# Optimization experiments

Hardware: AMD Instinct MI355X
Metric: run time of the kernel (lower is better)

## Reference

```python
import jax, jax.numpy as jnp
import numpy as np
from jax import lax

KH = KW = 3
STRIDE = 1
PAD = 1
B_COEF = 1.0
IN_CH = 64
OUT_CH = 64
C_LEN = 8
MLP_HIDDEN = 16


def setup_inputs() -> dict:
    key = jax.random.key(0)
    ks = jax.random.split(key, 8)
    IKK = IN_CH * KH * KW
    x = jax.random.normal(ks[0], (2, IN_CH, 32, 32), dtype=jnp.float32)
    c = jax.random.normal(ks[1], (2, C_LEN), dtype=jnp.float32)
    # static kernel [O, I*k*k] (xavier-uniform-ish)
    lim_k = float(np.sqrt(6.0 / (OUT_CH + IKK)))
    kernel = jax.random.uniform(ks[2], (OUT_CH, IKK), minval=-lim_k, maxval=lim_k, dtype=jnp.float32)
    bias = jax.random.normal(ks[3], (OUT_CH,), dtype=jnp.float32)
    # MLP: Linear(2+c_len -> 2*mlp_hidden), SiLU, Linear(2*mlp_hidden -> O*I*k*k)
    d_in = 2 + C_LEN
    d_h = 2 * MLP_HIDDEN
    lim1 = 0.1 * float(np.sqrt(6.0 / (d_in + d_h)))
    lim2 = 0.1 * float(np.sqrt(6.0 / (d_h + OUT_CH * IKK)))
    w1 = jax.random.uniform(ks[4], (d_in, d_h), minval=-lim1, maxval=lim1, dtype=jnp.float32)
    b1 = jnp.zeros((d_h,), dtype=jnp.float32)
    w2 = jax.random.uniform(ks[5], (d_h, OUT_CH * IKK), minval=-lim2, maxval=lim2, dtype=jnp.float32)
    b2 = jnp.zeros((OUT_CH * IKK,), dtype=jnp.float32)
    return {"x": x, "c": c, "kernel": kernel, "bias": bias, "w1": w1, "b1": b1, "w2": w2, "b2": b2}


def reference(x, c, kernel, bias, w1, b1, w2, b2):
    B, C, H, W = x.shape
    Ho = (H + 2 * PAD - KH) // STRIDE + 1
    Wo = (W + 2 * PAD - KW) // STRIDE + 1
    P = Ho * Wo
    O, IKK = kernel.shape
    # unfold: patches feature dim is channel-major (c, kh, kw), matching torch.nn.Unfold
    patches = lax.conv_general_dilated_patches(
        x, (KH, KW), (STRIDE, STRIDE), [(PAD, PAD), (PAD, PAD)])  # [B, IKK, Ho, Wo]
    xu = patches.reshape(B, IKK, P)  # [B, IKK, P]
    # normalized patch locations; ij-meshgrid over (x=W, y=H), flattened x-major (faithful to source)
    gx, gy = jnp.meshgrid(jnp.arange(Wo), jnp.arange(Ho), indexing='ij')
    locs = jnp.stack([gx / Wo, gy / Ho], axis=-1).reshape(-1, 2).astype(x.dtype)  # [P, 2]
    feat = jnp.concatenate(
        [jnp.broadcast_to(locs[None], (B, P, 2)),
         jnp.broadcast_to(c[:, None, :], (B, P, c.shape[1]))], axis=-1
    ).reshape(B * P, -1)  # [B*P, 2+c_len]
    h = jax.nn.silu(feat @ w1 + b1)
    adj = h @ w2 + b2  # [B*P, O*IKK]
    # faithful reshape (same raw-buffer reinterpretation as the torch .view)
    adj = adj.reshape(B, O, P, IKK).transpose(0, 1, 3, 2)  # [B, O, IKK, P]
    ak = kernel[None, :, :, None] + B_COEF * adj  # [B, O, IKK, P]
    out = jnp.einsum('bip,boip->bop', xu, ak)  # [B, O, P]
    out = out + bias[None, :, None]
    return out.reshape(B, O, Ho, Wo)
```

## Files before the change

### kernel.cpp

```cpp
#include <hip/hip_runtime.h>
#include <math.h>

#define CIN  64
#define HH   32
#define WW   32
#define OCH  64
#define IKK  576
#define DH   32
#define OIKK 36864

__device__ __forceinline__ float silu_f(float v) {
    return v / (1.0f + __expf(-v));
}

__global__ __launch_bounds__(256) void k_ts(const float* __restrict__ x,
                                            const float* __restrict__ w2,
                                            const float* __restrict__ b2,
                                            float* __restrict__ t_ws,
                                            float* __restrict__ s_ws) {
    __shared__ float patch[4][584];
    __shared__ float red[8][8][4][4];
    __shared__ float spart[4][64];
    int bid = blockIdx.x;
    int b   = bid >> 8;
    int q   = (bid >> 2) & 63;
    int ph  = bid & 3;
    int par = q >> 5, xq = q & 31;
    int tid = threadIdx.x;

    for (int idx = tid; idx < 4 * IKK; idx += 256) {
        int pgi = idx / IKK;
        int ikk = idx - pgi * IKK;
        int ci  = ikk / 9;
        int r   = ikk - ci * 9;
        int kh  = r / 3;
        int kw  = r - kh * 3;
        int yy  = 2 * (ph * 4 + pgi) + par + kh - 1;
        int xx  = xq + kw - 1;
        float v = 0.0f;
        if (yy >= 0 && yy < HH && xx >= 0 && xx < WW)
            v = x[((b * CIN + ci) * HH + yy) * WW + xx];
        patch[pgi][ikk] = v;
    }
    __syncthreads();

    int kq = tid >> 5;
    int jg = (tid >> 2) & 7;
    int pg = tid & 3;
    const float4* pr  = (const float4*)(&patch[pg][0]) + kq * 18;
    const float4* wp0 = (const float4*)(w2 + (size_t)(jg * 4 + 0) * OIKK + q * IKK) + kq * 18;
    const float4* wp1 = (const float4*)(w2 + (size_t)(jg * 4 + 1) * OIKK + q * IKK) + kq * 18;
    const float4* wp2 = (const float4*)(w2 + (size_t)(jg * 4 + 2) * OIKK + q * IKK) + kq * 18;
    const float4* wp3 = (const float4*)(w2 + (size_t)(jg * 4 + 3) * OIKK + q * IKK) + kq * 18;
    float4 a0 = {0,0,0,0}, a1 = {0,0,0,0}, a2 = {0,0,0,0}, a3 = {0,0,0,0};
    #pragma unroll 6
    for (int it = 0; it < 18; ++it) {
        float4 pv = pr[it];
        float4 w0 = wp0[it], w1v = wp1[it], w2v = wp2[it], w3v = wp3[it];
        a0.x = fmaf(w0.x, pv.x, a0.x); a0.y = fmaf(w0.y, pv.y, a0.y);
        a0.z = fmaf(w0.z, pv.z, a0.z); a0.w = fmaf(w0.w, pv.w, a0.w);
        a1.x = fmaf(w1v.x, pv.x, a1.x); a1.y = fmaf(w1v.y, pv.y, a1.y);
        a1.z = fmaf(w1v.z, pv.z, a1.z); a1.w = fmaf(w1v.w, pv.w, a1.w);
        a2.x = fmaf(w2v.x, pv.x, a2.x); a2.y = fmaf(w2v.y, pv.y, a2.y);
        a2.z = fmaf(w2v.z, pv.z, a2.z); a2.w = fmaf(w2v.w, pv.w, a2.w);
        a3.x = fmaf(w3v.x, pv.x, a3.x); a3.y = fmaf(w3v.y, pv.y, a3.y);
        a3.z = fmaf(w3v.z, pv.z, a3.z); a3.w = fmaf(w3v.w, pv.w, a3.w);
    }
    red[kq][jg][0][pg] = (a0.x + a0.y) + (a0.z + a0.w);
    red[kq][jg][1][pg] = (a1.x + a1.y) + (a1.z + a1.w);
    red[kq][jg][2][pg] = (a2.x + a2.y) + (a2.z + a2.w);
    red[kq][jg][3][pg] = (a3.x + a3.y) + (a3.z + a3.w);

    {
        int pix = tid >> 6, kc = tid & 63;
        const float* b2q = b2 + q * IKK + kc * 9;
        const float* pp  = &patch[pix][kc * 9];
        float acc = 0.f;
        #pragma unroll
        for (int i2 = 0; i2 < 9; ++i2) acc = fmaf(pp[i2], b2q[i2], acc);
        spart[pix][kc] = acc;
    }
    __syncthreads();

    if (tid < 128) {
        int j = tid >> 2, pg2 = tid & 3;
        int jg2 = j >> 2, jj2 = j & 3;
        float sum = 0.f;
        #pragma unroll
        for (int k = 0; k < 8; ++k) sum += red[k][jg2][jj2][pg2];
        int p = ((ph << 2) + pg2) * 64 + q;
        t_ws[(size_t)b * 32768 + (size_t)j * 1024 + p] = sum;
    }
    if (tid < 4) {
        float acc = 0.f;
        #pragma unroll
        for (int kc = 0; kc < 64; ++kc) acc += spart[tid][kc];
        s_ws[(b << 10) + ((ph << 2) + tid) * 64 + q] = acc;
    }
}

__global__ __launch_bounds__(256) void k_out(const float* __restrict__ x,
                                             const float* __restrict__ kern,
                                             const float* __restrict__ bias,
                                             const float* __restrict__ c,
                                             const float* __restrict__ w1,
                                             const float* __restrict__ b1,
                                             const float* __restrict__ t_ws,
                                             const float* __restrict__ s_ws,
                                             float* __restrict__ out) {
    __shared__ __align__(16) float xs[CIN][3][36];
    __shared__ __align__(16) float tl[DH][36];
    __shared__ float hl[16][33];
    __shared__ float sl[32];
    __shared__ float psum[2560];
    int bid = blockIdx.x;
    int b   = bid >> 7;
    int y   = (bid >> 2) & 31;
    int oc  = bid & 3;
    int tid = threadIdx.x;

    if (tid < 192) {
        int ci = tid / 3;
        int kh = tid - ci * 3;
        int yy = y + kh - 1;
        float4* dst = (float4*)(&xs[ci][kh][0]);
        if (yy >= 0 && yy < HH) {
            const float4* src = (const float4*)(x + ((b * CIN + ci) * HH + yy) * WW);
            float4 v[8];
            #pragma unroll
            for (int j = 0; j < 8; ++j) v[j] = src[j];
            dst[0] = make_float4(0.f, v[0].x, v[0].y, v[0].z);
            #pragma unroll
            for (int j = 1; j < 8; ++j)
                dst[j] = make_float4(v[j - 1].w, v[j].x, v[j].y, v[j].z);
            dst[8] = make_float4(v[7].w, 0.f, 0.f, 0.f);
        } else {
            float4 z = {0.f, 0.f, 0.f, 0.f};
            #pragma unroll
            for (int j = 0; j < 9; ++j) dst[j] = z;
        }
    }
    if (tid < 256) {
        int j = tid >> 3, g = tid & 7;
        float4 v = *(const float4*)(t_ws + (size_t)b * 32768 + (size_t)j * 1024 + (y << 5) + (g << 2));
        *(float4*)(&tl[j][g << 2]) = v;
    }
    for (int idx = tid; idx < 512; idx += 256) {
        int olx = idx >> 5, j = idx & 31;
        int o   = (oc << 4) + olx;
        int pm  = (o << 4) + (y >> 1);
        float f0 = (float)(pm >> 5) * (1.0f / 32.0f);
        float f1 = (float)(pm & 31) * (1.0f / 32.0f);
        float acc = b1[j];
        acc = fmaf(f0, w1[j], acc);
        acc = fmaf(f1, w1[DH + j], acc);
        #pragma unroll
        for (int i = 0; i < 8; ++i)
            acc = fmaf(c[(b << 3) + i], w1[(2 + i) * DH + j], acc);
        hl[olx][j] = silu_f(acc);
    }
    if (tid < 32) sl[tid] = s_ws[(b << 10) + (y << 5) + tid];
    __syncthreads();

    {
        int cq = tid >> 6;
        int ol = (tid >> 3) & 7;
        int xg = tid & 7;
        int o0 = (oc << 4) + ol;
        int o1 = o0 + 8;
        int ci0 = cq << 4;
        const float4* k0p = (const float4*)(kern + o0 * IKK + ci0 * 9);
        const float4* k1p = (const float4*)(kern + o1 * IKK + ci0 * 9);
        float aA[4] = {0.f, 0.f, 0.f, 0.f};
        float aB[4] = {0.f, 0.f, 0.f, 0.f};
        for (int c4 = 0; c4 < 4; ++c4) {
            float ka[36], kb[36];
            #pragma unroll
            for (int rr = 0; rr < 9; ++rr) {
                float4 va = k0p[c4 * 9 + rr];
                ka[rr * 4 + 0] = va.x; ka[rr * 4 + 1] = va.y;
                ka[rr * 4 + 2] = va.z; ka[rr * 4 + 3] = va.w;
                float4 vb = k1p[c4 * 9 + rr];
                kb[rr * 4 + 0] = vb.x; kb[rr * 4 + 1] = vb.y;
                kb[rr * 4 + 2] = vb.z; kb[rr * 4 + 3] = vb.w;
            }
            #pragma unroll
            for (int i = 0; i < 4; ++i) {
                int ci = ci0 + (c4 << 2) + i;
                #pragma unroll
                for (int kh = 0; kh < 3; ++kh) {
                    const float* row = &xs[ci][kh][0];
                    float4 v4 = *(const float4*)(row + 4 * xg);
                    float2 v2 = *(const float2*)(row + 4 * xg + 4);
                    int e = i * 9 + kh * 3;
                    float k0a = ka[e], k1a = ka[e + 1], k2a = ka[e + 2];
                    float k0b = kb[e], k1b = kb[e + 1], k2b = kb[e + 2];
                    aA[0] = fmaf(k0a, v4.x, aA[0]); aA[0] = fmaf(k1a, v4.y, aA[0]); aA[0] = fmaf(k2a, v4.z, aA[0]);
                    aA[1] = fmaf(k0a, v4.y, aA[1]); aA[1] = fmaf(k1a, v4.z, aA[1]); aA[1] = fmaf(k2a, v4.w, aA[1]);
                    aA[2] = fmaf(k0a, v4.z, aA[2]); aA[2] = fmaf(k1a, v4.w, aA[2]); aA[2] = fmaf(k2a, v2.x, aA[2]);
                    aA[3] = fmaf(k0a, v4.w, aA[3]); aA[3] = fmaf(k1a, v2.x, aA[3]); aA[3] = fmaf(k2a, v2.y, aA[3]);
                    aB[0] = fmaf(k0b, v4.x, aB[0]); aB[0] = fmaf(k1b, v4.y, aB[0]); aB[0] = fmaf(k2b, v4.z, aB[0]);
                    aB[1] = fmaf(k0b, v4.y, aB[1]); aB[1] = fmaf(k1b, v4.z, aB[1]); aB[1] = fmaf(k2b, v4.w, aB[1]);
                    aB[2] = fmaf(k0b, v4.z, aB[2]); aB[2] = fmaf(k1b, v4.w, aB[2]); aB[2] = fmaf(k2b, v2.x, aB[2]);
                    aB[3] = fmaf(k0b, v4.w, aB[3]); aB[3] = fmaf(k1b, v2.x, aB[3]); aB[3] = fmaf(k2b, v2.y, aB[3]);
                }
            }
        }
        float2* sp = (float2*)(psum + tid * 10);
        sp[0] = make_float2(aA[0], aA[1]);
        sp[1] = make_float2(aA[2], aA[3]);
        sp[2] = make_float2(aB[0], aB[1]);
        sp[3] = make_float2(aB[2], aB[3]);
    }
    __syncthreads();

    {
        int ou = tid >> 4;
        int xp = tid & 15;
        int o  = (oc << 4) + ou;
        int ol2 = ou & 7, oo = ou >> 3, xg2 = xp >> 1;
        int ppb = (xp & 1) << 1;
        float c0 = 0.f, c1 = 0.f;
        #pragma unroll
        for (int cq = 0; cq < 4; ++cq) {
            int t2 = (cq << 6) + (ol2 << 3) + xg2;
            float2 v = *(const float2*)(psum + t2 * 10 + (oo << 2) + ppb);
            c0 += v.x; c1 += v.y;
        }
        #pragma unroll 8
        for (int jj = 0; jj < DH; ++jj) {
            float2 tv = *(const float2*)(&tl[jj][2 * xp]);
            float hv = hl[ou][jj];
            c0 = fmaf(hv, tv.x, c0);
            c1 = fmaf(hv, tv.y, c1);
        }
        float bo = bias[o];
        int base = ((b * OCH + o) << 10) + (y << 5) + 2 * xp;
        *(float2*)(out + base) = make_float2(c0 + bo + sl[2 * xp], c1 + bo + sl[2 * xp + 1]);
    }
}

extern "C" void kernel_launch(void* const* d_in, const int* in_sizes, int n_in,
                              void* d_out, int out_size, void* d_ws, size_t ws_size,
                              hipStream_t stream) {
    const float* x    = (const float*)d_in[0];
    const float* c    = (const float*)d_in[1];
    const float* kern = (const float*)d_in[2];
    const float* bias = (const float*)d_in[3];
    const float* w1   = (const float*)d_in[4];
    const float* b1   = (const float*)d_in[5];
    const float* w2   = (const float*)d_in[6];
    const float* b2   = (const float*)d_in[7];
    float* out  = (float*)d_out;
    float* t_ws = (float*)d_ws;
    float* s_ws = t_ws + 65536;

    k_ts <<<512, 256, 0, stream>>>(x, w2, b2, t_ws, s_ws);
    k_out<<<256, 256, 0, stream>>>(x, kern, bias, c, w1, b1, t_ws, s_ws, out);
}
```

Measured before the change: 22.26 us.

## Fuse both kernels into one launch with a global atomic flag dependency

Merges the t/s-projection kernel and the output kernel into a single 768-block launch. The output blocks run their static-kernel convolution first, then spin on a device-scope counter until all 512 producer blocks have published, and only then consume the workspace. The goal is to remove the gap between two kernel launches and overlap the static convolution with the producer work. The cost is an extra memset per call and a spin-wait that relies on all producer blocks being scheduled, with block ordering helping to avoid deadlock.

```diff
diff --git a/kernel.cpp b/kernel.cpp
--- a/kernel.cpp
+++ b/kernel.cpp
@@ -8,235 +8,251 @@
 #define IKK  576
 #define DH   32
 #define OIKK 36864
+#define NTS  512
+
+struct TsSmem {
+    float patch[4][584];
+    float red[8][8][4][4];
+    float spart[4][64];
+};
+struct OutSmem {
+    float xs[CIN][3][36];
+    float tl[DH][36];
+    float hl[16][33];
+    float sl[32];
+    float psum[2560];
+};
+union Smem { TsSmem ts; OutSmem ot; };
 
 __device__ __forceinline__ float silu_f(float v) {
     return v / (1.0f + __expf(-v));
 }
 
-__global__ __launch_bounds__(256) void k_ts(const float* __restrict__ x,
-                                            const float* __restrict__ w2,
-                                            const float* __restrict__ b2,
-                                            float* __restrict__ t_ws,
-                                            float* __restrict__ s_ws) {
-    __shared__ float patch[4][584];
-    __shared__ float red[8][8][4][4];
-    __shared__ float spart[4][64];
+__global__ __launch_bounds__(256, 2) void k_fused(
+    const float* __restrict__ x, const float* __restrict__ c,
+    const float* __restrict__ kern, const float* __restrict__ bias,
+    const float* __restrict__ w1, const float* __restrict__ b1,
+    const float* __restrict__ w2, const float* __restrict__ b2,
+    float* __restrict__ t_ws, float* __restrict__ s_ws,
+    unsigned int* __restrict__ flag, float* __restrict__ out)
+{
+    __shared__ Smem sm;
+    int tid = threadIdx.x;
     int bid = blockIdx.x;
-    int b   = bid >> 8;
-    int q   = (bid >> 2) & 63;
-    int ph  = bid & 3;
-    int par = q >> 5, xq = q & 31;
-    int tid = threadIdx.x;
-
-    for (int idx = tid; idx < 4 * IKK; idx += 256) {
-        int pgi = idx / IKK;
-        int ikk = idx - pgi * IKK;
-        int ci  = ikk / 9;
-        int r   = ikk - ci * 9;
-        int kh  = r / 3;
-        int kw  = r - kh * 3;
-        int yy  = 2 * (ph * 4 + pgi) + par + kh - 1;
-        int xx  = xq + kw - 1;
-        float v = 0.0f;
-        if (yy >= 0 && yy < HH && xx >= 0 && xx < WW)
-            v = x[((b * CIN + ci) * HH + yy) * WW + xx];
-        patch[pgi][ikk] = v;
-    }
-    __syncthreads();
-
-    int kq = tid >> 5;
-    int jg = (tid >> 2) & 7;
-    int pg = tid & 3;
-    const float4* pr  = (const float4*)(&patch[pg][0]) + kq * 18;
-    const float4* wp0 = (const float4*)(w2 + (size_t)(jg * 4 + 0) * OIKK + q * IKK) + kq * 18;
-    const float4* wp1 = (const float4*)(w2 + (size_t)(jg * 4 + 1) * OIKK + q * IKK) + kq * 18;
-    const float4* wp2 = (const float4*)(w2 + (size_t)(jg * 4 + 2) * OIKK + q * IKK) + kq * 18;
-    const float4* wp3 = (const float4*)(w2 + (size_t)(jg * 4 + 3) * OIKK + q * IKK) + kq * 18;
-    float4 a0 = {0,0,0,0}, a1 = {0,0,0,0}, a2 = {0,0,0,0}, a3 = {0,0,0,0};
-    #pragma unroll 6
-    for (int it = 0; it < 18; ++it) {
-        float4 pv = pr[it];
-        float4 w0 = wp0[it], w1v = wp1[it], w2v = wp2[it], w3v = wp3[it];
-        a0.x = fmaf(w0.x, pv.x, a0.x); a0.y = fmaf(w0.y, pv.y, a0.y);
-        a0.z = fmaf(w0.z, pv.z, a0.z); a0.w = fmaf(w0.w, pv.w, a0.w);
-        a1.x = fmaf(w1v.x, pv.x, a1.x); a1.y = fmaf(w1v.y, pv.y, a1.y);
-        a1.z = fmaf(w1v.z, pv.z, a1.z); a1.w = fmaf(w1v.w, pv.w, a1.w);
-        a2.x = fmaf(w2v.x, pv.x, a2.x); a2.y = fmaf(w2v.y, pv.y, a2.y);
-        a2.z = fmaf(w2v.z, pv.z, a2.z); a2.w = fmaf(w2v.w, pv.w, a2.w);
-        a3.x = fmaf(w3v.x, pv.x, a3.x); a3.y = fmaf(w3v.y, pv.y, a3.y);
-        a3.z = fmaf(w3v.z, pv.z, a3.z); a3.w = fmaf(w3v.w, pv.w, a3.w);
-    }
-    red[kq][jg][0][pg] = (a0.x + a0.y) + (a0.z + a0.w);
-    red[kq][jg][1][pg] = (a1.x + a1.y) + (a1.z + a1.w);
-    red[kq][jg][2][pg] = (a2.x + a2.y) + (a2.z + a2.w);
-    red[kq][jg][3][pg] = (a3.x + a3.y) + (a3.z + a3.w);
-
-    {
-        int pix = tid >> 6, kc = tid & 63;
-        const float* b2q = b2 + q * IKK + kc * 9;
-        const float* pp  = &patch[pix][kc * 9];
-        float acc = 0.f;
-        #pragma unroll
-        for (int i2 = 0; i2 < 9; ++i2) acc = fmaf(pp[i2], b2q[i2], acc);
-        spart[pix][kc] = acc;
-    }
-    __syncthreads();
-
-    if (tid < 128) {
-        int j = tid >> 2, pg2 = tid & 3;
-        int jg2 = j >> 2, jj2 = j & 3;
-        float sum = 0.f;
-        #pragma unroll
-        for (int k = 0; k < 8; ++k) sum += red[k][jg2][jj2][pg2];
-        int p = ((ph << 2) + pg2) * 64 + q;
-        t_ws[(size_t)b * 32768 + (size_t)j * 1024 + p] = sum;
-    }
-    if (tid < 4) {
-        float acc = 0.f;
-        #pragma unroll
-        for (int kc = 0; kc < 64; ++kc) acc += spart[tid][kc];
-        s_ws[(b << 10) + ((ph << 2) + tid) * 64 + q] = acc;
-    }
-}
-
-__global__ __launch_bounds__(256) void k_out(const float* __restrict__ x,
-                                             const float* __restrict__ kern,
-                                             const float* __restrict__ bias,
-                                             const float* __restrict__ c,
-                                             const float* __restrict__ w1,
-                                             const float* __restrict__ b1,
-                                             const float* __restrict__ t_ws,
-                                             const float* __restrict__ s_ws,
-                                             float* __restrict__ out) {
-    __shared__ __align__(16) float xs[CIN][3][36];
-    __shared__ __align__(16) float tl[DH][36];
-    __shared__ float hl[16][33];
-    __shared__ float sl[32];
-    __shared__ float psum[2560];
-    int bid = blockIdx.x;
-    int b   = bid >> 7;
-    int y   = (bid >> 2) & 31;
-    int oc  = bid & 3;
-    int tid = threadIdx.x;
-
-    if (tid < 192) {
-        int ci = tid / 3;
-        int kh = tid - ci * 3;
-        int yy = y + kh - 1;
-        float4* dst = (float4*)(&xs[ci][kh][0]);
-        if (yy >= 0 && yy < HH) {
-            const float4* src = (const float4*)(x + ((b * CIN + ci) * HH + yy) * WW);
-            float4 v[8];
-            #pragma unroll
-            for (int j = 0; j < 8; ++j) v[j] = src[j];
-            dst[0] = make_float4(0.f, v[0].x, v[0].y, v[0].z);
-            #pragma unroll
-            for (int j = 1; j < 8; ++j)
-                dst[j] = make_float4(v[j - 1].w, v[j].x, v[j].y, v[j].z);
-            dst[8] = make_float4(v[7].w, 0.f, 0.f, 0.f);
-        } else {
-            float4 z = {0.f, 0.f, 0.f, 0.f};
-            #pragma unroll
-            for (int j = 0; j < 9; ++j) dst[j] = z;
-        }
-    }
-    if (tid < 256) {
-        int j = tid >> 3, g = tid & 7;
-        float4 v = *(const float4*)(t_ws + (size_t)b * 32768 + (size_t)j * 1024 + (y << 5) + (g << 2));
-        *(float4*)(&tl[j][g << 2]) = v;
-    }
-    for (int idx = tid; idx < 512; idx += 256) {
-        int olx = idx >> 5, j = idx & 31;
-        int o   = (oc << 4) + olx;
-        int pm  = (o << 4) + (y >> 1);
-        float f0 = (float)(pm >> 5) * (1.0f / 32.0f);
-        float f1 = (float)(pm & 31) * (1.0f / 32.0f);
-        float acc = b1[j];
-        acc = fmaf(f0, w1[j], acc);
-        acc = fmaf(f1, w1[DH + j], acc);
-        #pragma unroll
-        for (int i = 0; i < 8; ++i)
-            acc = fmaf(c[(b << 3) + i], w1[(2 + i) * DH + j], acc);
-        hl[olx][j] = silu_f(acc);
-    }
-    if (tid < 32) sl[tid] = s_ws[(b << 10) + (y << 5) + tid];
-    __syncthreads();
-
-    {
-        int cq = tid >> 6;
-        int ol = (tid >> 3) & 7;
-        int xg = tid & 7;
-        int o0 = (oc << 4) + ol;
-        int o1 = o0 + 8;
-        int ci0 = cq << 4;
-        const float4* k0p = (const float4*)(kern + o0 * IKK + ci0 * 9);
-        const float4* k1p = (const float4*)(kern + o1 * IKK + ci0 * 9);
-        float aA[4] = {0.f, 0.f, 0.f, 0.f};
-        float aB[4] = {0.f, 0.f, 0.f, 0.f};
-        for (int c4 = 0; c4 < 4; ++c4) {
-            float ka[36], kb[36];
-            #pragma unroll
-            for (int rr = 0; rr < 9; ++rr) {
-                float4 va = k0p[c4 * 9 + rr];
-                ka[rr * 4 + 0] = va.x; ka[rr * 4 + 1] = va.y;
-                ka[rr * 4 + 2] = va.z; ka[rr * 4 + 3] = va.w;
-                float4 vb = k1p[c4 * 9 + rr];
-                kb[rr * 4 + 0] = vb.x; kb[rr * 4 + 1] = vb.y;
-                kb[rr * 4 + 2] = vb.z; kb[rr * 4 + 3] = vb.w;
-            }
-            #pragma unroll
-            for (int i = 0; i < 4; ++i) {
-                int ci = ci0 + (c4 << 2) + i;
-                #pragma unroll
-                for (int kh = 0; kh < 3; ++kh) {
-                    const float* row = &xs[ci][kh][0];
-                    float4 v4 = *(const float4*)(row + 4 * xg);
-                    float2 v2 = *(const float2*)(row + 4 * xg + 4);
-                    int e = i * 9 + kh * 3;
-                    float k0a = ka[e], k1a = ka[e + 1], k2a = ka[e + 2];
-                    float k0b = kb[e], k1b = kb[e + 1], k2b = kb[e + 2];
-                    aA[0] = fmaf(k0a, v4.x, aA[0]); aA[0] = fmaf(k1a, v4.y, aA[0]); aA[0] = fmaf(k2a, v4.z, aA[0]);
-                    aA[1] = fmaf(k0a, v4.y, aA[1]); aA[1] = fmaf(k1a, v4.z, aA[1]); aA[1] = fmaf(k2a, v4.w, aA[1]);
-                    aA[2] = fmaf(k0a, v4.z, aA[2]); aA[2] = fmaf(k1a, v4.w, aA[2]); aA[2] = fmaf(k2a, v2.x, aA[2]);
-                    aA[3] = fmaf(k0a, v4.w, aA[3]); aA[3] = fmaf(k1a, v2.x, aA[3]); aA[3] = fmaf(k2a, v2.y, aA[3]);
-                    aB[0] = fmaf(k0b, v4.x, aB[0]); aB[0] = fmaf(k1b, v4.y, aB[0]); aB[0] = fmaf(k2b, v4.z, aB[0]);
-                    aB[1] = fmaf(k0b, v4.y, aB[1]); aB[1] = fmaf(k1b, v4.z, aB[1]); aB[1] = fmaf(k2b, v4.w, aB[1]);
-                    aB[2] = fmaf(k0b, v4.z, aB[2]); aB[2] = fmaf(k1b, v4.w, aB[2]); aB[2] = fmaf(k2b, v2.x, aB[2]);
-                    aB[3] = fmaf(k0b, v4.w, aB[3]); aB[3] = fmaf(k1b, v2.x, aB[3]); aB[3] = fmaf(k2b, v2.y, aB[3]);
+
+    if (bid < NTS) {
+        int b   = bid >> 8;
+        int q   = (bid >> 2) & 63;
+        int ph  = bid & 3;
+        int par = q >> 5, xq = q & 31;
+
+        for (int idx = tid; idx < 4 * IKK; idx += 256) {
+            int pgi = idx / IKK;
+            int ikk = idx - pgi * IKK;
+            int ci  = ikk / 9;
+            int r   = ikk - ci * 9;
+            int kh  = r / 3;
+            int kw  = r - kh * 3;
+            int yy  = 2 * (ph * 4 + pgi) + par + kh - 1;
+            int xx  = xq + kw - 1;
+            float v = 0.0f;
+            if (yy >= 0 && yy < HH && xx >= 0 && xx < WW)
+                v = x[((b * CIN + ci) * HH + yy) * WW + xx];
+            sm.ts.patch[pgi][ikk] = v;
+        }
+        __syncthreads();
+
+        int kq = tid >> 5;
+        int jg = (tid >> 2) & 7;
+        int pg = tid & 3;
+        const float4* pr  = (const float4*)(&sm.ts.patch[pg][0]) + kq * 18;
+        const float4* wp0 = (const float4*)(w2 + (size_t)(jg * 4 + 0) * OIKK + q * IKK) + kq * 18;
+        const float4* wp1 = (const float4*)(w2 + (size_t)(jg * 4 + 1) * OIKK + q * IKK) + kq * 18;
+        const float4* wp2 = (const float4*)(w2 + (size_t)(jg * 4 + 2) * OIKK + q * IKK) + kq * 18;
+        const float4* wp3 = (const float4*)(w2 + (size_t)(jg * 4 + 3) * OIKK + q * IKK) + kq * 18;
+        float4 a0 = {0,0,0,0}, a1 = {0,0,0,0}, a2 = {0,0,0,0}, a3 = {0,0,0,0};
+        #pragma unroll 6
+        for (int it = 0; it < 18; ++it) {
+            float4 pv = pr[it];
+            float4 w0 = wp0[it], w1v = wp1[it], w2v = wp2[it], w3v = wp3[it];
+            a0.x = fmaf(w0.x, pv.x, a0.x); a0.y = fmaf(w0.y, pv.y, a0.y);
+            a0.z = fmaf(w0.z, pv.z, a0.z); a0.w = fmaf(w0.w, pv.w, a0.w);
+            a1.x = fmaf(w1v.x, pv.x, a1.x); a1.y = fmaf(w1v.y, pv.y, a1.y);
+            a1.z = fmaf(w1v.z, pv.z, a1.z); a1.w = fmaf(w1v.w, pv.w, a1.w);
+            a2.x = fmaf(w2v.x, pv.x, a2.x); a2.y = fmaf(w2v.y, pv.y, a2.y);
+            a2.z = fmaf(w2v.z, pv.z, a2.z); a2.w = fmaf(w2v.w, pv.w, a2.w);
+            a3.x = fmaf(w3v.x, pv.x, a3.x); a3.y = fmaf(w3v.y, pv.y, a3.y);
+            a3.z = fmaf(w3v.z, pv.z, a3.z); a3.w = fmaf(w3v.w, pv.w, a3.w);
+        }
+        sm.ts.red[kq][jg][0][pg] = (a0.x + a0.y) + (a0.z + a0.w);
+        sm.ts.red[kq][jg][1][pg] = (a1.x + a1.y) + (a1.z + a1.w);
+        sm.ts.red[kq][jg][2][pg] = (a2.x + a2.y) + (a2.z + a2.w);
+        sm.ts.red[kq][jg][3][pg] = (a3.x + a3.y) + (a3.z + a3.w);
+
+        {
+            int pix = tid >> 6, kc = tid & 63;
+            const float* b2q = b2 + q * IKK + kc * 9;
+            const float* pp  = &sm.ts.patch[pix][kc * 9];
+            float acc = 0.f;
+            #pragma unroll
+            for (int i2 = 0; i2 < 9; ++i2) acc = fmaf(pp[i2], b2q[i2], acc);
+            sm.ts.spart[pix][kc] = acc;
+        }
+        __syncthreads();
+
+        if (tid < 128) {
+            int j = tid >> 2, pg2 = tid & 3;
+            int jg2 = j >> 2, jj2 = j & 3;
+            float sum = 0.f;
+            #pragma unroll
+            for (int k = 0; k < 8; ++k) sum += sm.ts.red[k][jg2][jj2][pg2];
+            int p = ((ph << 2) + pg2) * 64 + q;
+            t_ws[(size_t)b * 32768 + (size_t)j * 1024 + p] = sum;
+        }
+        if (tid < 4) {
+            float acc = 0.f;
+            #pragma unroll
+            for (int kc = 0; kc < 64; ++kc) acc += sm.ts.spart[tid][kc];
+            s_ws[(b << 10) + ((ph << 2) + tid) * 64 + q] = acc;
+        }
+        __syncthreads();
+        if (tid == 0) {
+            __threadfence();
+            __hip_atomic_fetch_add(flag, 1u, __ATOMIC_RELEASE, __HIP_MEMORY_SCOPE_AGENT);
+        }
+    } else {
+        int obid = bid - NTS;
+        int b   = obid >> 7;
+        int y   = (obid >> 2) & 31;
+        int oc  = obid & 3;
+
+        if (tid < 192) {
+            int ci = tid / 3;
+            int kh = tid - ci * 3;
+            int yy = y + kh - 1;
+            float4* dst = (float4*)(&sm.ot.xs[ci][kh][0]);
+            if (yy >= 0 && yy < HH) {
+                const float4* src = (const float4*)(x + ((b * CIN + ci) * HH + yy) * WW);
+                float4 v[8];
+                #pragma unroll
+                for (int j = 0; j < 8; ++j) v[j] = src[j];
+                dst[0] = make_float4(0.f, v[0].x, v[0].y, v[0].z);
+                #pragma unroll
+                for (int j = 1; j < 8; ++j)
+                    dst[j] = make_float4(v[j - 1].w, v[j].x, v[j].y, v[j].z);
+                dst[8] = make_float4(v[7].w, 0.f, 0.f, 0.f);
+            } else {
+                float4 z = {0.f, 0.f, 0.f, 0.f};
+                #pragma unroll
+                for (int j = 0; j < 9; ++j) dst[j] = z;
+            }
+        }
+        for (int idx = tid; idx < 512; idx += 256) {
+            int olx = idx >> 5, j = idx & 31;
+            int o   = (oc << 4) + olx;
+            int pm  = (o << 4) + (y >> 1);
+            float f0 = (float)(pm >> 5) * (1.0f / 32.0f);
+            float f1 = (float)(pm & 31) * (1.0f / 32.0f);
+            float acc = b1[j];
+            acc = fmaf(f0, w1[j], acc);
+            acc = fmaf(f1, w1[DH + j], acc);
+            #pragma unroll
+            for (int i = 0; i < 8; ++i)
+                acc = fmaf(c[(b << 3) + i], w1[(2 + i) * DH + j], acc);
+            sm.ot.hl[olx][j] = silu_f(acc);
+        }
+        __syncthreads();
+
+        {
+            int cq = tid >> 6;
+            int ol = (tid >> 3) & 7;
+            int xg = tid & 7;
+            int o0 = (oc << 4) + ol;
+            int o1 = o0 + 8;
+            int ci0 = cq << 4;
+            const float4* k0p = (const float4*)(kern + o0 * IKK + ci0 * 9);
+            const float4* k1p = (const float4*)(kern + o1 * IKK + ci0 * 9);
+            float aA[4] = {0.f, 0.f, 0.f, 0.f};
+            float aB[4] = {0.f, 0.f, 0.f, 0.f};
+            for (int c4 = 0; c4 < 4; ++c4) {
+                float ka[36], kb[36];
+                #pragma unroll
+                for (int rr = 0; rr < 9; ++rr) {
+                    float4 va = k0p[c4 * 9 + rr];
+                    ka[rr * 4 + 0] = va.x; ka[rr * 4 + 1] = va.y;
+                    ka[rr * 4 + 2] = va.z; ka[rr * 4 + 3] = va.w;
+                    float4 vb = k1p[c4 * 9 + rr];
+                    kb[rr * 4 + 0] = vb.x; kb[rr * 4 + 1] = vb.y;
+                    kb[rr * 4 + 2] = vb.z; kb[rr * 4 + 3] = vb.w;
                 }
-            }
-        }
-        float2* sp = (float2*)(psum + tid * 10);
-        sp[0] = make_float2(aA[0], aA[1]);
-        sp[1] = make_float2(aA[2], aA[3]);
-        sp[2] = make_float2(aB[0], aB[1]);
-        sp[3] = make_float2(aB[2], aB[3]);
-    }
-    __syncthreads();
-
-    {
-        int ou = tid >> 4;
-        int xp = tid & 15;
-        int o  = (oc << 4) + ou;
-        int ol2 = ou & 7, oo = ou >> 3, xg2 = xp >> 1;
-        int ppb = (xp & 1) << 1;
-        float c0 = 0.f, c1 = 0.f;
-        #pragma unroll
-        for (int cq = 0; cq < 4; ++cq) {
-            int t2 = (cq << 6) + (ol2 << 3) + xg2;
-            float2 v = *(const float2*)(psum + t2 * 10 + (oo << 2) + ppb);
-            c0 += v.x; c1 += v.y;
-        }
-        #pragma unroll 8
-        for (int jj = 0; jj < DH; ++jj) {
-            float2 tv = *(const float2*)(&tl[jj][2 * xp]);
-            float hv = hl[ou][jj];
-            c0 = fmaf(hv, tv.x, c0);
-            c1 = fmaf(hv, tv.y, c1);
-        }
-        float bo = bias[o];
-        int base = ((b * OCH + o) << 10) + (y << 5) + 2 * xp;
-        *(float2*)(out + base) = make_float2(c0 + bo + sl[2 * xp], c1 + bo + sl[2 * xp + 1]);
+                #pragma unroll
+                for (int i = 0; i < 4; ++i) {
+                    int ci = ci0 + (c4 << 2) + i;
+                    #pragma unroll
+                    for (int kh = 0; kh < 3; ++kh) {
+                        const float* row = &sm.ot.xs[ci][kh][0];
+                        float4 v4 = *(const float4*)(row + 4 * xg);
+                        float2 v2 = *(const float2*)(row + 4 * xg + 4);
+                        int e = i * 9 + kh * 3;
+                        float k0a = ka[e], k1a = ka[e + 1], k2a = ka[e + 2];
+                        float k0b = kb[e], k1b = kb[e + 1], k2b = kb[e + 2];
+                        aA[0] = fmaf(k0a, v4.x, aA[0]); aA[0] = fmaf(k1a, v4.y, aA[0]); aA[0] = fmaf(k2a, v4.z, aA[0]);
+                        aA[1] = fmaf(k0a, v4.y, aA[1]); aA[1] = fmaf(k1a, v4.z, aA[1]); aA[1] = fmaf(k2a, v4.w, aA[1]);
+                        aA[2] = fmaf(k0a, v4.z, aA[2]); aA[2] = fmaf(k1a, v4.w, aA[2]); aA[2] = fmaf(k2a, v2.x, aA[2]);
+                        aA[3] = fmaf(k0a, v4.w, aA[3]); aA[3] = fmaf(k1a, v2.x, aA[3]); aA[3] = fmaf(k2a, v2.y, aA[3]);
+                        aB[0] = fmaf(k0b, v4.x, aB[0]); aB[0] = fmaf(k1b, v4.y, aB[0]); aB[0] = fmaf(k2b, v4.z, aB[0]);
+                        aB[1] = fmaf(k0b, v4.y, aB[1]); aB[1] = fmaf(k1b, v4.z, aB[1]); aB[1] = fmaf(k2b, v4.w, aB[1]);
+                        aB[2] = fmaf(k0b, v4.z, aB[2]); aB[2] = fmaf(k1b, v4.w, aB[2]); aB[2] = fmaf(k2b, v2.x, aB[2]);
+                        aB[3] = fmaf(k0b, v4.w, aB[3]); aB[3] = fmaf(k1b, v2.x, aB[3]); aB[3] = fmaf(k2b, v2.y, aB[3]);
+                    }
+                }
+            }
+            float2* sp = (float2*)(sm.ot.psum + tid * 10);
+            sp[0] = make_float2(aA[0], aA[1]);
+            sp[1] = make_float2(aA[2], aA[3]);
+            sp[2] = make_float2(aB[0], aB[1]);
+            sp[3] = make_float2(aB[2], aB[3]);
+        }
+
+        if (tid == 0) {
+            while (__hip_atomic_load(flag, __ATOMIC_ACQUIRE, __HIP_MEMORY_SCOPE_AGENT) < NTS)
+                __builtin_amdgcn_s_sleep(1);
+        }
+        __syncthreads();
+
+        {
+            int j = tid >> 3, g = tid & 7;
+            float4 v = *(const float4*)(t_ws + (size_t)b * 32768 + (size_t)j * 1024 + (y << 5) + (g << 2));
+            *(float4*)(&sm.ot.tl[j][g << 2]) = v;
+        }
+        if (tid < 32) sm.ot.sl[tid] = s_ws[(b << 10) + (y << 5) + tid];
+        __syncthreads();
+
+        {
+            int ou = tid >> 4;
+            int xp = tid & 15;
+            int o  = (oc << 4) + ou;
+            int ol2 = ou & 7, oo = ou >> 3, xg2 = xp >> 1;
+            int ppb = (xp & 1) << 1;
+            float c0 = 0.f, c1 = 0.f;
+            #pragma unroll
+            for (int cq = 0; cq < 4; ++cq) {
+                int t2 = (cq << 6) + (ol2 << 3) + xg2;
+                float2 v = *(const float2*)(sm.ot.psum + t2 * 10 + (oo << 2) + ppb);
+                c0 += v.x; c1 += v.y;
+            }
+            #pragma unroll 8
+            for (int jj = 0; jj < DH; ++jj) {
+                float2 tv = *(const float2*)(&sm.ot.tl[jj][2 * xp]);
+                float hv = sm.ot.hl[ou][jj];
+                c0 = fmaf(hv, tv.x, c0);
+                c1 = fmaf(hv, tv.y, c1);
+            }
+            float bo = bias[o];
+            int base = ((b * OCH + o) << 10) + (y << 5) + 2 * xp;
+            *(float2*)(out + base) = make_float2(c0 + bo + sm.ot.sl[2 * xp],
+                                                 c1 + bo + sm.ot.sl[2 * xp + 1]);
+        }
     }
 }
 
@@ -254,7 +270,9 @@
     float* out  = (float*)d_out;
     float* t_ws = (float*)d_ws;
     float* s_ws = t_ws + 65536;
-
-    k_ts <<<512, 256, 0, stream>>>(x, w2, b2, t_ws, s_ws);
-    k_out<<<256, 256, 0, stream>>>(x, kern, bias, c, w1, b1, t_ws, s_ws, out);
+    unsigned int* flag = (unsigned int*)(s_ws + 2048);
+
+    hipMemsetAsync((void*)flag, 0, 4, stream);
+    k_fused<<<768, 256, 0, stream>>>(x, c, kern, bias, w1, b1, w2, b2,
+                                     t_ws, s_ws, flag, out);
 }
```

Result: slower. 81.18 us (+264.7%).
